# Kernel optimization log

Hardware: AMD Instinct MI355X
Metric: run time of the kernel (lower is better)

The kernel has to match this reference:

```python
import jax, jax.numpy as jnp
import numpy as np

K = 3          # kernel size
STRIDE = 1
PAD = 1
DIL = 1
BN_EPS = 1e-5


def _conv2d(x, w, b, stride=STRIDE, pad=PAD):
    out = jax.lax.conv_general_dilated(
        x, w, (stride, stride), [(pad, pad), (pad, pad)],
        dimension_numbers=("NCHW", "OIHW", "NCHW"))
    return out + b[None, :, None, None]


def _bilinear_sample(x, py, px):
    """Zero-padded bilinear sampling. x: [B,C,H,W]; py,px: [B,Ho,Wo] float coords."""
    B, C, H, W = x.shape
    y0 = jnp.floor(py)
    x0 = jnp.floor(px)
    wy1 = py - y0
    wx1 = px - x0
    x_flat = x.reshape(B, C, H * W)

    def gather(yi, xi, wgt):
        valid = (yi >= 0) & (yi <= H - 1) & (xi >= 0) & (xi <= W - 1)
        yc = jnp.clip(yi, 0, H - 1).astype(jnp.int32)
        xc = jnp.clip(xi, 0, W - 1).astype(jnp.int32)
        idx = (yc * W + xc).reshape(B, 1, -1)                      # [B,1,Ho*Wo]
        v = jnp.take_along_axis(x_flat, idx, axis=2)               # [B,C,Ho*Wo]
        v = v.reshape(B, C, py.shape[1], py.shape[2])
        return v * (wgt * valid)[:, None]

    return (gather(y0,     x0,     (1 - wy1) * (1 - wx1)) +
            gather(y0,     x0 + 1, (1 - wy1) * wx1) +
            gather(y0 + 1, x0,     wy1 * (1 - wx1)) +
            gather(y0 + 1, x0 + 1, wy1 * wx1))


def _forward(x, off_w, off_b, dc_w, dc_b, bn_gamma, bn_beta, bn_mean, bn_var):
    B, C, H, W = x.shape
    K2 = K * K
    om = _conv2d(x, off_w, off_b)                 # [B, 3*K2, H, W]
    offset = om[:, :2 * K2]                       # interleaved (dy, dx) per tap
    mask = jax.nn.sigmoid(om[:, 2 * K2:])         # [B, K2, H, W]

    # output pixel -> top-left input coordinate of the receptive field
    base_y = (jnp.arange(H) * STRIDE - PAD)[:, None]   # [H,1]
    base_x = (jnp.arange(W) * STRIDE - PAD)[None, :]   # [1,W]

    out = jnp.zeros((B, dc_w.shape[0], H, W), dtype=x.dtype)
    for k in range(K2):
        kh, kw = k // K, k % K
        py = base_y + kh * DIL + offset[:, 2 * k]      # [B,H,W]
        px = base_x + kw * DIL + offset[:, 2 * k + 1]  # [B,H,W]
        samp = _bilinear_sample(x, py, px) * mask[:, k][:, None]
        out = out + jnp.einsum('oc,bchw->bohw', dc_w[:, :, kh, kw], samp)
    out = out + dc_b[None, :, None, None]

    # BatchNorm (inference: running stats) + ReLU
    scale = bn_gamma / jnp.sqrt(bn_var + BN_EPS)
    out = out * scale[None, :, None, None] + (bn_beta - bn_mean * scale)[None, :, None, None]
    return jax.nn.relu(out)


def setup_inputs() -> dict:
    key = jax.random.key(0)
    ks = jax.random.split(key, 8)
    B, Cin, Cout, H, W = 8, 256, 256, 64, 64
    K2 = K * K
    x = jax.random.normal(ks[0], (B, Cin, H, W), dtype=jnp.float32)
    # NOTE: original init zeros the offset conv; we use small random weights so
    # offsets/masks are nontrivial and the bilinear path is exercised.
    off_w = jax.random.normal(ks[1], (3 * K2, Cin, K, K), dtype=jnp.float32) * 0.01
    off_b = jax.random.normal(ks[2], (3 * K2,), dtype=jnp.float32) * 0.01
    dc_w = jax.random.normal(ks[3], (Cout, Cin, K, K), dtype=jnp.float32) / np.sqrt(Cin * K2)
    dc_b = jax.random.normal(ks[4], (Cout,), dtype=jnp.float32) * 0.01
    bn_gamma = jnp.ones((Cout,), dtype=jnp.float32)
    bn_beta = jnp.zeros((Cout,), dtype=jnp.float32)
    bn_mean = jax.random.normal(ks[5], (Cout,), dtype=jnp.float32) * 0.1
    bn_var = jax.random.uniform(ks[6], (Cout,), dtype=jnp.float32) * 0.5 + 0.5
    return {"x": x, "off_w": off_w, "off_b": off_b, "dc_w": dc_w, "dc_b": dc_b,
            "bn_gamma": bn_gamma, "bn_beta": bn_beta,
            "bn_mean": bn_mean, "bn_var": bn_var}


def reference(x, off_w, off_b, dc_w, dc_b, bn_gamma, bn_beta, bn_mean, bn_var):
    return _forward(x, off_w, off_b, dc_w, dc_b, bn_gamma, bn_beta, bn_mean, bn_var)
```

## Files before the change

### kernel.cpp

```cpp
#include <hip/hip_runtime.h>
#include <hip/hip_bf16.h>
#include <hip/hip_fp16.h>
#include <cstdint>
#include <cstddef>

#define HH 64
#define WW 64
#define CIN 256
#define COUT 256
#define NB 8
#define HW (HH * WW)
#define BN_EPS 1e-5f

typedef __attribute__((ext_vector_type(8))) short s16x8;
typedef __attribute__((ext_vector_type(8))) unsigned short u16x8;
typedef __attribute__((ext_vector_type(4))) float f32x4;

static __device__ __forceinline__ float bf2f(unsigned short u) {
  unsigned int v = ((unsigned int)u) << 16;
  return __builtin_bit_cast(float, v);
}
static __device__ __forceinline__ unsigned short f2bf(float f) {
  __hip_bfloat16 h = __float2bfloat16(f);
  return __builtin_bit_cast(unsigned short, h);
}

__global__ __launch_bounds__(256) void k_tr(const float* __restrict__ x,
                                            unsigned short* __restrict__ xbf) {
  __shared__ float tile[64][65];
  int bid = blockIdx.x;
  int b = bid & 7;
  int r = bid >> 3;
  int ct = r & 3;
  int st = r >> 2;
  int lane = threadIdx.x & 63;
  int grp = threadIdx.x >> 6;
  int c0 = ct * 64, s0 = st * 64;
  const float* xb = x + (size_t)b * CIN * HW;
#pragma unroll
  for (int i = 0; i < 16; ++i) {
    int row = grp * 16 + i;
    tile[row][lane] = xb[(size_t)(c0 + row) * HW + s0 + lane];
  }
  __syncthreads();
  unsigned short* xo = xbf + (size_t)b * HW * CIN;
#pragma unroll
  for (int i = 0; i < 16; ++i) {
    int row = grp * 16 + i;
    xo[(size_t)(s0 + row) * CIN + c0 + lane] = f2bf(tile[lane][row]);
  }
}

__global__ __launch_bounds__(256) void k_wt(const float* __restrict__ dc_w,
                                            unsigned short* __restrict__ Wf) {
  int idx = blockIdx.x * 256 + threadIdx.x;
  if (idx >= 9 * 8 * 16 * 64 * 8) return;
  int j = idx & 7;
  int lane = (idx >> 3) & 63;
  int tile = (idx >> 9) & 15;
  int ks = (idx >> 13) & 7;
  int k = idx >> 16;
  int o = tile * 16 + (lane & 15);
  int c = ks * 32 + (lane >> 4) * 8 + j;
  Wf[idx] = f2bf(dc_w[((size_t)o * CIN + c) * 9 + k]);
}

__global__ __launch_bounds__(256) void k_owt(const float* __restrict__ off_w,
                                             unsigned short* __restrict__ OWf) {
  int idx = blockIdx.x * 256 + threadIdx.x;
  if (idx >= 9 * 8 * 2 * 64 * 8) return;
  int j = idx & 7;
  int lane = (idx >> 3) & 63;
  int kot = (idx >> 9) & 1;
  int ks = (idx >> 10) & 7;
  int t = idx >> 13;
  int ko = kot * 16 + (lane & 15);
  int c = ks * 32 + (lane >> 4) * 8 + j;
  unsigned short v = 0;
  if (ko < 27) v = f2bf(off_w[((size_t)ko * CIN + c) * 9 + t]);
  OWf[idx] = v;
}

__global__ void k_bn(const float* __restrict__ g, const float* __restrict__ be,
                     const float* __restrict__ m, const float* __restrict__ va,
                     const float* __restrict__ db, float* __restrict__ sc,
                     float* __restrict__ bi) {
  int o = threadIdx.x;
  float s = g[o] * rsqrtf(va[o] + BN_EPS);
  sc[o] = s;
  bi[o] = be[o] + (db[o] - m[o]) * s;
}

__global__ __launch_bounds__(256, 4) void k_main(
    const unsigned short* __restrict__ xbf, const unsigned short* __restrict__ OWf,
    const float* __restrict__ off_b, const unsigned short* __restrict__ Wf,
    const float* __restrict__ bnsc, const float* __restrict__ bnbi,
    float* __restrict__ out) {
  int bid = blockIdx.x;
  int b = bid & 7;
  int r = bid >> 3;
  int h = r & 63;
  int q = r >> 6;
  int wq = q * 32;
  int tid = threadIdx.x;
  int lane = tid & 63;
  int wave = tid >> 6;
  int l15 = lane & 15, l4 = lane >> 4;

  __shared__ __align__(16) unsigned short ubuf[34 * 256];
  __shared__ float om_lds[27][32];
  __shared__ unsigned short pre_offS[9][32][4];
  __shared__ __half pre_wH[9][32][4];

  const unsigned short* xb = xbf + (size_t)b * HW * CIN;

  f32x4 acc_oc[2];
  acc_oc[0] = (f32x4){0.f, 0.f, 0.f, 0.f};
  acc_oc[1] = (f32x4){0.f, 0.f, 0.f, 0.f};
  int ptile = wave & 1;
  int gstart = wq - 1;

  for (int kh = 0; kh < 3; ++kh) {
    int y = h + kh - 1;
    if (y < 0 || y >= HH) continue;
    __syncthreads();
    const unsigned short* srow = xb + (size_t)y * WW * CIN;
    for (int e = tid; e < 34 * 32; e += 256) {
      int col = e >> 5;
      int ch = e & 31;
      int g = gstart + col;
      u16x8 v = {0, 0, 0, 0, 0, 0, 0, 0};
      if (g >= 0 && g < WW) v = *(const u16x8*)(srow + (size_t)g * CIN + ch * 8);
      *(u16x8*)&ubuf[col * 256 + ((ch ^ (col & 7)) * 8)] = v;
    }
    __syncthreads();
    if (wave < 2) {
#pragma unroll
      for (int kw = 0; kw < 3; ++kw) {
        int prow = ptile * 16 + l15 + kw;
        int rs = prow & 7;
        const unsigned short* Atap =
            OWf + ((size_t)(kh * 3 + kw) * 8) * 1024 + lane * 8;
#pragma unroll
        for (int ks = 0; ks < 8; ++ks) {
          s16x8 bfrag = *(const s16x8*)&ubuf[prow * 256 + (((ks * 4 + l4) ^ rs) * 8)];
#pragma unroll
          for (int kot = 0; kot < 2; ++kot) {
            s16x8 afrag = *(const s16x8*)(Atap + ks * 1024 + kot * 512);
            acc_oc[kot] = __builtin_amdgcn_mfma_f32_16x16x32_bf16(afrag, bfrag,
                                                                  acc_oc[kot], 0, 0, 0);
          }
        }
      }
    }
  }
  if (wave < 2) {
#pragma unroll
    for (int kot = 0; kot < 2; ++kot) {
#pragma unroll
      for (int j = 0; j < 4; ++j) {
        int ko = kot * 16 + l4 * 4 + j;
        if (ko < 27) om_lds[ko][ptile * 16 + l15] = acc_oc[kot][j];
      }
    }
  }
  __syncthreads();

  for (int item = tid; item < 9 * 32; item += 256) {
    int k = item >> 5;
    int wl = item & 31;
    int w = wq + wl;
    int kh = k / 3, kw = k % 3;
    float offy = om_lds[2 * k][wl] + off_b[2 * k];
    float offx = om_lds[2 * k + 1][wl] + off_b[2 * k + 1];
    float mk = om_lds[18 + k][wl] + off_b[18 + k];
    mk = 1.0f / (1.0f + expf(-mk));
    float py = (float)(h - 1 + kh) + offy;
    float px = (float)(w - 1 + kw) + offx;
    float fy0 = floorf(py), fx0 = floorf(px);
    float wy1 = py - fy0, wx1 = px - fx0;
    int y0 = (int)fy0, x0 = (int)fx0;
    int y1 = y0 + 1, x1 = x0 + 1;
    bool vy0 = (y0 >= 0) && (y0 <= HH - 1);
    bool vy1 = (y1 >= 0) && (y1 <= HH - 1);
    bool vx0 = (x0 >= 0) && (x0 <= WW - 1);
    bool vx1 = (x1 >= 0) && (x1 <= WW - 1);
    int y0c = min(max(y0, 0), HH - 1), y1c = min(max(y1, 0), HH - 1);
    int x0c = min(max(x0, 0), WW - 1), x1c = min(max(x1, 0), WW - 1);
    pre_wH[k][wl][0] =
        __float2half((1.f - wy1) * (1.f - wx1) * mk * ((vy0 && vx0) ? 1.f : 0.f));
    pre_wH[k][wl][1] = __float2half((1.f - wy1) * wx1 * mk * ((vy0 && vx1) ? 1.f : 0.f));
    pre_wH[k][wl][2] = __float2half(wy1 * (1.f - wx1) * mk * ((vy1 && vx0) ? 1.f : 0.f));
    pre_wH[k][wl][3] = __float2half(wy1 * wx1 * mk * ((vy1 && vx1) ? 1.f : 0.f));
    pre_offS[k][wl][0] = (unsigned short)(y0c * WW + x0c);
    pre_offS[k][wl][1] = (unsigned short)(y0c * WW + x1c);
    pre_offS[k][wl][2] = (unsigned short)(y1c * WW + x0c);
    pre_offS[k][wl][3] = (unsigned short)(y1c * WW + x1c);
  }

  unsigned short(*S)[256] = (unsigned short(*)[256])ubuf;
  f32x4 acc[4][2];
#pragma unroll
  for (int i = 0; i < 4; ++i)
#pragma unroll
    for (int j = 0; j < 2; ++j) acc[i][j] = (f32x4){0.f, 0.f, 0.f, 0.f};

  int o_base = wave * 64;
  int hv = lane >> 5;
  int chunk = lane & 31;

  for (int k = 0; k < 9; ++k) {
    __syncthreads();
    {
#pragma unroll
      for (int pp = 0; pp < 4; ++pp) {
        int pl = wave * 8 + pp * 2 + hv;
        int i0 = ((int)pre_offS[k][pl][0]) << 8;
        int i1 = ((int)pre_offS[k][pl][1]) << 8;
        int i2 = ((int)pre_offS[k][pl][2]) << 8;
        int i3 = ((int)pre_offS[k][pl][3]) << 8;
        float w0 = __half2float(pre_wH[k][pl][0]);
        float w1 = __half2float(pre_wH[k][pl][1]);
        float w2 = __half2float(pre_wH[k][pl][2]);
        float w3 = __half2float(pre_wH[k][pl][3]);
        u16x8 v0 = *(const u16x8*)(xb + i0 + chunk * 8);
        u16x8 v1 = *(const u16x8*)(xb + i1 + chunk * 8);
        u16x8 v2 = *(const u16x8*)(xb + i2 + chunk * 8);
        u16x8 v3 = *(const u16x8*)(xb + i3 + chunk * 8);
        u16x8 rr;
#pragma unroll
        for (int j = 0; j < 8; ++j) {
          float s = w0 * bf2f(v0[j]) + w1 * bf2f(v1[j]) + w2 * bf2f(v2[j]) +
                    w3 * bf2f(v3[j]);
          rr[j] = f2bf(s);
        }
        int phys = chunk ^ (pl & 7);
        *(u16x8*)&S[pl][phys * 8] = rr;
      }
    }
    __syncthreads();
    const unsigned short* Wa = Wf + (size_t)k * 65536 + (wave * 4) * 512 + lane * 8;
#pragma unroll
    for (int ks = 0; ks < 8; ++ks) {
      s16x8 a[4], bf[2];
#pragma unroll
      for (int ot = 0; ot < 4; ++ot)
        a[ot] = *(const s16x8*)(Wa + ks * 8192 + ot * 512);
#pragma unroll
      for (int pt = 0; pt < 2; ++pt) {
        int pl = pt * 16 + l15;
        int slot = (ks * 4 + l4) ^ (pl & 7);
        bf[pt] = *(const s16x8*)&S[pl][slot * 8];
      }
#pragma unroll
      for (int ot = 0; ot < 4; ++ot)
#pragma unroll
        for (int pt = 0; pt < 2; ++pt)
          acc[ot][pt] = __builtin_amdgcn_mfma_f32_16x16x32_bf16(a[ot], bf[pt],
                                                                acc[ot][pt], 0, 0, 0);
    }
  }

#pragma unroll
  for (int ot = 0; ot < 4; ++ot) {
#pragma unroll
    for (int j = 0; j < 4; ++j) {
      int o = o_base + ot * 16 + l4 * 4 + j;
      float sc = bnsc[o], bi = bnbi[o];
      float* ob = out + (((size_t)b * COUT + o) * HH + h) * WW + wq;
#pragma unroll
      for (int pt = 0; pt < 2; ++pt) {
        ob[pt * 16 + l15] = fmaxf(fmaf(acc[ot][pt][j], sc, bi), 0.f);
      }
    }
  }
}

extern "C" void kernel_launch(void* const* d_in, const int* in_sizes, int n_in,
                              void* d_out, int out_size, void* d_ws, size_t ws_size,
                              hipStream_t stream) {
  const float* x = (const float*)d_in[0];
  const float* off_w = (const float*)d_in[1];
  const float* off_b = (const float*)d_in[2];
  const float* dc_w = (const float*)d_in[3];
  const float* dc_b = (const float*)d_in[4];
  const float* bn_gamma = (const float*)d_in[5];
  const float* bn_beta = (const float*)d_in[6];
  const float* bn_mean = (const float*)d_in[7];
  const float* bn_var = (const float*)d_in[8];
  float* out = (float*)d_out;

  char* ws = (char*)d_ws;
  unsigned short* xbf = (unsigned short*)ws;
  ws += (size_t)NB * HW * CIN * sizeof(unsigned short);
  unsigned short* Wf = (unsigned short*)ws;
  ws += (size_t)9 * 8 * 16 * 64 * 8 * sizeof(unsigned short);
  unsigned short* OWf = (unsigned short*)ws;
  ws += (size_t)9 * 8 * 2 * 64 * 8 * sizeof(unsigned short);
  float* bnsc = (float*)ws;
  ws += 256 * sizeof(float);
  float* bnbi = (float*)ws;

  k_tr<<<NB * 64 * 4, 256, 0, stream>>>(x, xbf);
  k_wt<<<(9 * 8 * 16 * 64 * 8 + 255) / 256, 256, 0, stream>>>(dc_w, Wf);
  k_owt<<<(9 * 8 * 2 * 64 * 8 + 255) / 256, 256, 0, stream>>>(off_w, OWf);
  k_bn<<<1, 256, 0, stream>>>(bn_gamma, bn_beta, bn_mean, bn_var, dc_b, bnsc, bnbi);
  k_main<<<NB * HH * 2, 256, 0, stream>>>(xbf, OWf, off_b, Wf, bnsc, bnbi, out);
}
```

Measured before the change: 106.2 us.

## Double-buffer sampled tile and prefetch next tap's gathers during MFMA

The per-tap loop now keeps two LDS buffers for the sampled tile. Each iteration issues the global gathers for tap k+1 into registers before the MFMA phase of tap k, which hides gather latency and leaves one barrier per tap instead of two. The A and B fragments in the MFMA loop are software-pipelined with double-buffered registers, and the sampling offsets and weights are packed into a single uint4 per pixel. The extra live registers (16 u16x8 gathers plus the fragment buffers) cost occupancy, so launch bounds drop from 4 to 2 blocks per SM.

```diff
diff --git a/kernel.cpp b/kernel.cpp
--- a/kernel.cpp
+++ b/kernel.cpp
@@ -23,6 +23,9 @@
 static __device__ __forceinline__ unsigned short f2bf(float f) {
   __hip_bfloat16 h = __float2bfloat16(f);
   return __builtin_bit_cast(unsigned short, h);
+}
+static __device__ __forceinline__ float h2f(unsigned short u) {
+  return __half2float(__builtin_bit_cast(__half, u));
 }
 
 __global__ __launch_bounds__(256) void k_tr(const float* __restrict__ x,
@@ -91,7 +94,7 @@
   bi[o] = be[o] + (db[o] - m[o]) * s;
 }
 
-__global__ __launch_bounds__(256, 4) void k_main(
+__global__ __launch_bounds__(256, 2) void k_main(
     const unsigned short* __restrict__ xbf, const unsigned short* __restrict__ OWf,
     const float* __restrict__ off_b, const unsigned short* __restrict__ Wf,
     const float* __restrict__ bnsc, const float* __restrict__ bnbi,
@@ -107,10 +110,9 @@
   int wave = tid >> 6;
   int l15 = lane & 15, l4 = lane >> 4;
 
-  __shared__ __align__(16) unsigned short ubuf[34 * 256];
+  __shared__ __align__(16) unsigned short pool[64 * 256];
   __shared__ float om_lds[27][32];
-  __shared__ unsigned short pre_offS[9][32][4];
-  __shared__ __half pre_wH[9][32][4];
+  __shared__ uint4 pre_pack[9][32];
 
   const unsigned short* xb = xbf + (size_t)b * HW * CIN;
 
@@ -131,7 +133,7 @@
       int g = gstart + col;
       u16x8 v = {0, 0, 0, 0, 0, 0, 0, 0};
       if (g >= 0 && g < WW) v = *(const u16x8*)(srow + (size_t)g * CIN + ch * 8);
-      *(u16x8*)&ubuf[col * 256 + ((ch ^ (col & 7)) * 8)] = v;
+      *(u16x8*)&pool[col * 256 + ((ch ^ (col & 7)) * 8)] = v;
     }
     __syncthreads();
     if (wave < 2) {
@@ -143,7 +145,7 @@
             OWf + ((size_t)(kh * 3 + kw) * 8) * 1024 + lane * 8;
 #pragma unroll
         for (int ks = 0; ks < 8; ++ks) {
-          s16x8 bfrag = *(const s16x8*)&ubuf[prow * 256 + (((ks * 4 + l4) ^ rs) * 8)];
+          s16x8 bfrag = *(const s16x8*)&pool[prow * 256 + (((ks * 4 + l4) ^ rs) * 8)];
 #pragma unroll
           for (int kot = 0; kot < 2; ++kot) {
             s16x8 afrag = *(const s16x8*)(Atap + ks * 1024 + kot * 512);
@@ -187,18 +189,25 @@
     bool vx1 = (x1 >= 0) && (x1 <= WW - 1);
     int y0c = min(max(y0, 0), HH - 1), y1c = min(max(y1, 0), HH - 1);
     int x0c = min(max(x0, 0), WW - 1), x1c = min(max(x1, 0), WW - 1);
-    pre_wH[k][wl][0] =
-        __float2half((1.f - wy1) * (1.f - wx1) * mk * ((vy0 && vx0) ? 1.f : 0.f));
-    pre_wH[k][wl][1] = __float2half((1.f - wy1) * wx1 * mk * ((vy0 && vx1) ? 1.f : 0.f));
-    pre_wH[k][wl][2] = __float2half(wy1 * (1.f - wx1) * mk * ((vy1 && vx0) ? 1.f : 0.f));
-    pre_wH[k][wl][3] = __float2half(wy1 * wx1 * mk * ((vy1 && vx1) ? 1.f : 0.f));
-    pre_offS[k][wl][0] = (unsigned short)(y0c * WW + x0c);
-    pre_offS[k][wl][1] = (unsigned short)(y0c * WW + x1c);
-    pre_offS[k][wl][2] = (unsigned short)(y1c * WW + x0c);
-    pre_offS[k][wl][3] = (unsigned short)(y1c * WW + x1c);
-  }
-
-  unsigned short(*S)[256] = (unsigned short(*)[256])ubuf;
+    float w0 = (1.f - wy1) * (1.f - wx1) * mk * ((vy0 && vx0) ? 1.f : 0.f);
+    float w1 = (1.f - wy1) * wx1 * mk * ((vy0 && vx1) ? 1.f : 0.f);
+    float w2 = wy1 * (1.f - wx1) * mk * ((vy1 && vx0) ? 1.f : 0.f);
+    float w3 = wy1 * wx1 * mk * ((vy1 && vx1) ? 1.f : 0.f);
+    unsigned int i0 = (unsigned)(y0c * WW + x0c), i1 = (unsigned)(y0c * WW + x1c);
+    unsigned int i2 = (unsigned)(y1c * WW + x0c), i3 = (unsigned)(y1c * WW + x1c);
+    unsigned int h0 = __builtin_bit_cast(unsigned short, __float2half(w0));
+    unsigned int h1 = __builtin_bit_cast(unsigned short, __float2half(w1));
+    unsigned int h2 = __builtin_bit_cast(unsigned short, __float2half(w2));
+    unsigned int h3 = __builtin_bit_cast(unsigned short, __float2half(w3));
+    uint4 pk;
+    pk.x = i0 | (i1 << 16);
+    pk.y = i2 | (i3 << 16);
+    pk.z = h0 | (h1 << 16);
+    pk.w = h2 | (h3 << 16);
+    pre_pack[k][wl] = pk;
+  }
+  __syncthreads();
+
   f32x4 acc[4][2];
 #pragma unroll
   for (int i = 0; i < 4; ++i)
@@ -209,56 +218,82 @@
   int hv = lane >> 5;
   int chunk = lane & 31;
 
+  u16x8 g[4][4];
+  uint4 pr[4];
+
+  auto issue_k = [&](int kk) {
+#pragma unroll
+    for (int pp = 0; pp < 4; ++pp) {
+      int pl = wave * 8 + pp * 2 + hv;
+      uint4 pk = pre_pack[kk][pl];
+      pr[pp] = pk;
+      g[pp][0] = *(const u16x8*)(xb + ((pk.x & 0xffffu) << 8) + chunk * 8);
+      g[pp][1] = *(const u16x8*)(xb + ((pk.x >> 16) << 8) + chunk * 8);
+      g[pp][2] = *(const u16x8*)(xb + ((pk.y & 0xffffu) << 8) + chunk * 8);
+      g[pp][3] = *(const u16x8*)(xb + ((pk.y >> 16) << 8) + chunk * 8);
+    }
+  };
+
+  int cur = 0;
+  issue_k(0);
+
   for (int k = 0; k < 9; ++k) {
-    __syncthreads();
-    {
-#pragma unroll
-      for (int pp = 0; pp < 4; ++pp) {
-        int pl = wave * 8 + pp * 2 + hv;
-        int i0 = ((int)pre_offS[k][pl][0]) << 8;
-        int i1 = ((int)pre_offS[k][pl][1]) << 8;
-        int i2 = ((int)pre_offS[k][pl][2]) << 8;
-        int i3 = ((int)pre_offS[k][pl][3]) << 8;
-        float w0 = __half2float(pre_wH[k][pl][0]);
-        float w1 = __half2float(pre_wH[k][pl][1]);
-        float w2 = __half2float(pre_wH[k][pl][2]);
-        float w3 = __half2float(pre_wH[k][pl][3]);
-        u16x8 v0 = *(const u16x8*)(xb + i0 + chunk * 8);
-        u16x8 v1 = *(const u16x8*)(xb + i1 + chunk * 8);
-        u16x8 v2 = *(const u16x8*)(xb + i2 + chunk * 8);
-        u16x8 v3 = *(const u16x8*)(xb + i3 + chunk * 8);
-        u16x8 rr;
-#pragma unroll
-        for (int j = 0; j < 8; ++j) {
-          float s = w0 * bf2f(v0[j]) + w1 * bf2f(v1[j]) + w2 * bf2f(v2[j]) +
-                    w3 * bf2f(v3[j]);
-          rr[j] = f2bf(s);
+    unsigned short* Sc = pool + cur * (32 * 256);
+#pragma unroll
+    for (int pp = 0; pp < 4; ++pp) {
+      int pl = wave * 8 + pp * 2 + hv;
+      float w0 = h2f((unsigned short)(pr[pp].z & 0xffffu));
+      float w1 = h2f((unsigned short)(pr[pp].z >> 16));
+      float w2 = h2f((unsigned short)(pr[pp].w & 0xffffu));
+      float w3 = h2f((unsigned short)(pr[pp].w >> 16));
+      u16x8 rr;
+#pragma unroll
+      for (int j = 0; j < 8; ++j) {
+        float s = w0 * bf2f(g[pp][0][j]) + w1 * bf2f(g[pp][1][j]) +
+                  w2 * bf2f(g[pp][2][j]) + w3 * bf2f(g[pp][3][j]);
+        rr[j] = f2bf(s);
+      }
+      int phys = chunk ^ (pl & 7);
+      *(u16x8*)&Sc[pl * 256 + phys * 8] = rr;
+    }
+    if (k < 8) issue_k(k + 1);
+    asm volatile("s_waitcnt lgkmcnt(0)" ::: "memory");
+    __builtin_amdgcn_s_barrier();
+    __builtin_amdgcn_sched_barrier(0);
+
+    const unsigned short* Wa = Wf + (size_t)k * 65536 + (wave * 4) * 512 + lane * 8;
+    s16x8 aR[2][4];
+    s16x8 bR[2][2];
+#pragma unroll
+    for (int ot = 0; ot < 4; ++ot) aR[0][ot] = *(const s16x8*)(Wa + ot * 512);
+#pragma unroll
+    for (int pt = 0; pt < 2; ++pt) {
+      int pl = pt * 16 + l15;
+      int slot = l4 ^ (pl & 7);
+      bR[0][pt] = *(const s16x8*)&Sc[pl * 256 + slot * 8];
+    }
+#pragma unroll
+    for (int ks = 0; ks < 8; ++ks) {
+      int cb = ks & 1, nb = cb ^ 1;
+      if (ks < 7) {
+#pragma unroll
+        for (int ot = 0; ot < 4; ++ot)
+          aR[nb][ot] = *(const s16x8*)(Wa + (ks + 1) * 8192 + ot * 512);
+#pragma unroll
+        for (int pt = 0; pt < 2; ++pt) {
+          int pl = pt * 16 + l15;
+          int slot = ((ks + 1) * 4 + l4) ^ (pl & 7);
+          bR[nb][pt] = *(const s16x8*)&Sc[pl * 256 + slot * 8];
         }
-        int phys = chunk ^ (pl & 7);
-        *(u16x8*)&S[pl][phys * 8] = rr;
-      }
-    }
-    __syncthreads();
-    const unsigned short* Wa = Wf + (size_t)k * 65536 + (wave * 4) * 512 + lane * 8;
-#pragma unroll
-    for (int ks = 0; ks < 8; ++ks) {
-      s16x8 a[4], bf[2];
+      }
 #pragma unroll
       for (int ot = 0; ot < 4; ++ot)
-        a[ot] = *(const s16x8*)(Wa + ks * 8192 + ot * 512);
-#pragma unroll
-      for (int pt = 0; pt < 2; ++pt) {
-        int pl = pt * 16 + l15;
-        int slot = (ks * 4 + l4) ^ (pl & 7);
-        bf[pt] = *(const s16x8*)&S[pl][slot * 8];
-      }
-#pragma unroll
-      for (int ot = 0; ot < 4; ++ot)
 #pragma unroll
         for (int pt = 0; pt < 2; ++pt)
-          acc[ot][pt] = __builtin_amdgcn_mfma_f32_16x16x32_bf16(a[ot], bf[pt],
+          acc[ot][pt] = __builtin_amdgcn_mfma_f32_16x16x32_bf16(aR[cb][ot], bR[cb][pt],
                                                                 acc[ot][pt], 0, 0, 0);
     }
+    cur ^= 1;
   }
 
 #pragma unroll
```

Result: slower. 141.7 us (+33.5%).

## Stagger block start with s_sleep and pack bilinear blend into paired FMAs

Applied to the files above, without the earlier changes.

Rewrites the per-pixel bilinear blend to unpack bf16 pairs from 32-bit words, accumulate with two-wide float FMAs, and convert back with a single packed v_cvt_pk_bf16_f32. The aim is fewer scalar convert and FMA instructions in the sampling stage. It also adds a barrier and a block-dependent s_sleep delay so blocks start their main loop at staggered times, meant to spread out gather and weight-load bursts. The stagger idles some blocks for a while, and the inline asm assumes the target supports that conversion instruction.

```diff
diff --git a/kernel.cpp b/kernel.cpp
--- a/kernel.cpp
+++ b/kernel.cpp
@@ -15,6 +15,8 @@
 typedef __attribute__((ext_vector_type(8))) short s16x8;
 typedef __attribute__((ext_vector_type(8))) unsigned short u16x8;
 typedef __attribute__((ext_vector_type(4))) float f32x4;
+typedef __attribute__((ext_vector_type(2))) float f32x2;
+typedef __attribute__((ext_vector_type(4))) unsigned int u32x4;
 
 static __device__ __forceinline__ float bf2f(unsigned short u) {
   unsigned int v = ((unsigned int)u) << 16;
@@ -197,6 +199,12 @@
     pre_offS[k][wl][2] = (unsigned short)(y1c * WW + x0c);
     pre_offS[k][wl][3] = (unsigned short)(y1c * WW + x1c);
   }
+  __syncthreads();
+
+  {
+    int slot = ((bid >> 3) ^ (bid >> 8)) & 3;
+    for (int i = 0; i < slot; ++i) __builtin_amdgcn_s_sleep(25);
+  }
 
   unsigned short(*S)[256] = (unsigned short(*)[256])ubuf;
   f32x4 acc[4][2];
@@ -223,19 +231,32 @@
         float w1 = __half2float(pre_wH[k][pl][1]);
         float w2 = __half2float(pre_wH[k][pl][2]);
         float w3 = __half2float(pre_wH[k][pl][3]);
-        u16x8 v0 = *(const u16x8*)(xb + i0 + chunk * 8);
-        u16x8 v1 = *(const u16x8*)(xb + i1 + chunk * 8);
-        u16x8 v2 = *(const u16x8*)(xb + i2 + chunk * 8);
-        u16x8 v3 = *(const u16x8*)(xb + i3 + chunk * 8);
-        u16x8 rr;
-#pragma unroll
-        for (int j = 0; j < 8; ++j) {
-          float s = w0 * bf2f(v0[j]) + w1 * bf2f(v1[j]) + w2 * bf2f(v2[j]) +
-                    w3 * bf2f(v3[j]);
-          rr[j] = f2bf(s);
+        u32x4 m0 = __builtin_bit_cast(u32x4, *(const u16x8*)(xb + i0 + chunk * 8));
+        u32x4 m1 = __builtin_bit_cast(u32x4, *(const u16x8*)(xb + i1 + chunk * 8));
+        u32x4 m2 = __builtin_bit_cast(u32x4, *(const u16x8*)(xb + i2 + chunk * 8));
+        u32x4 m3 = __builtin_bit_cast(u32x4, *(const u16x8*)(xb + i3 + chunk * 8));
+        f32x2 w0p = {w0, w0}, w1p = {w1, w1}, w2p = {w2, w2}, w3p = {w3, w3};
+        u32x4 ro;
+#pragma unroll
+        for (int s = 0; s < 4; ++s) {
+          f32x2 t0 = {bf2f((unsigned short)(m0[s] & 0xffffu)),
+                      __builtin_bit_cast(float, m0[s] & 0xffff0000u)};
+          f32x2 t1 = {bf2f((unsigned short)(m1[s] & 0xffffu)),
+                      __builtin_bit_cast(float, m1[s] & 0xffff0000u)};
+          f32x2 t2 = {bf2f((unsigned short)(m2[s] & 0xffffu)),
+                      __builtin_bit_cast(float, m2[s] & 0xffff0000u)};
+          f32x2 t3 = {bf2f((unsigned short)(m3[s] & 0xffffu)),
+                      __builtin_bit_cast(float, m3[s] & 0xffff0000u)};
+          f32x2 a2 = t0 * w0p;
+          a2 = __builtin_elementwise_fma(t1, w1p, a2);
+          a2 = __builtin_elementwise_fma(t2, w2p, a2);
+          a2 = __builtin_elementwise_fma(t3, w3p, a2);
+          unsigned int o;
+          asm("v_cvt_pk_bf16_f32 %0, %1, %2" : "=v"(o) : "v"(a2[0]), "v"(a2[1]));
+          ro[s] = o;
         }
         int phys = chunk ^ (pl & 7);
-        *(u16x8*)&S[pl][phys * 8] = rr;
+        *(u16x8*)&S[pl][phys * 8] = __builtin_bit_cast(u16x8, ro);
       }
     }
     __syncthreads();
```

Measured after the change: 106.4 us. About the same (+0.2%).
